# Optimization experiments

Hardware: AMD Instinct MI355X
Metric: run time of the kernel (lower is better)

Reference implementation:

```python
import jax, jax.numpy as jnp
import numpy as np

N_HEAD = 16

def setup_inputs() -> dict:
    key = jax.random.key(0)
    ks = jax.random.split(key, 5)
    B, S, C = 4, 2048, 1024
    x = jax.random.normal(ks[0], (B, S, C), dtype=jnp.float32)
    w_qkv = jax.random.normal(ks[1], (C, 3 * C), dtype=jnp.float32) * (1.0 / np.sqrt(C))
    b_qkv = jnp.zeros((3 * C,), dtype=jnp.float32)
    w_proj = jax.random.normal(ks[2], (C, C), dtype=jnp.float32) * (1.0 / np.sqrt(C))
    b_proj = jnp.zeros((C,), dtype=jnp.float32)
    return {"x": x, "w_qkv": w_qkv, "b_qkv": b_qkv, "w_proj": w_proj, "b_proj": b_proj}

def reference(x, w_qkv, b_qkv, w_proj, b_proj):
    B, S, C = x.shape
    H = N_HEAD
    D = C // H
    qkv = x @ w_qkv + b_qkv                       # [B,S,3C]
    q, k, v = jnp.split(qkv, 3, axis=-1)
    # [B,S,C] -> [B,H,S,D]
    q = q.reshape(B, S, H, D).transpose(0, 2, 1, 3)
    k = k.reshape(B, S, H, D).transpose(0, 2, 1, 3)
    v = v.reshape(B, S, H, D).transpose(0, 2, 1, 3)
    scores = jnp.einsum('bhqd,bhkd->bhqk', q, k) / jnp.sqrt(jnp.float32(D))
    causal = jnp.tril(jnp.ones((S, S), dtype=bool))
    scores = jnp.where(causal[None, None], scores, -jnp.inf)
    weights = jax.nn.softmax(scores, axis=-1)     # dropout p=0 -> identity
    out = jnp.einsum('bhqk,bhkd->bhqd', weights, v)
    out = out.transpose(0, 2, 1, 3).reshape(B, S, C)
    return out @ w_proj + b_proj
```

## Files before the change

kernel.cpp:

```cpp
#include <hip/hip_runtime.h>

#define SDIM 2048
#define CDIM 1024
#define BDIM 4
#define HDIM 16
#define DDIM 64

#define ATT_SCALE 0.18033688011112042f

typedef __attribute__((ext_vector_type(8))) short bf16x8;
typedef __attribute__((ext_vector_type(4))) short bf16x4;
typedef __attribute__((ext_vector_type(4))) float f32x4;
typedef unsigned short u16;

#define MFMA __builtin_amdgcn_mfma_f32_16x16x32_bf16
#define LDS_ORDER_FENCE() __asm__ __volatile__("" ::: "memory")

#define TILE_BAR()                                                            \
    LDS_ORDER_FENCE();                                                        \
    __builtin_amdgcn_s_barrier();                                             \
    LDS_ORDER_FENCE()

__device__ __forceinline__ u16 f2b(float f) {
    union { float f; unsigned u; } v; v.f = f;
    unsigned r = v.u + 0x7FFFu + ((v.u >> 16) & 1u);
    return (u16)(r >> 16);
}
__device__ __forceinline__ u16 f2b_trunc(float f) {
    union { float f; unsigned u; } v; v.f = f;
    return (u16)(v.u >> 16);
}

typedef const __attribute__((address_space(1))) unsigned int* gas_t;
typedef __attribute__((address_space(3))) unsigned int* las_t;
__device__ __forceinline__ void cp16(const void* g, void* l) {
    __builtin_amdgcn_global_load_lds((gas_t)g, (las_t)l, 16, 0, 0);
}

__device__ __forceinline__ float fast_exp2(float x) {
#if __has_builtin(__builtin_amdgcn_exp2f)
    return __builtin_amdgcn_exp2f(x);
#else
    return __exp2f(x);
#endif
}

__global__ __launch_bounds__(256) void prep(
    const float* __restrict__ x, const float* __restrict__ w_qkv,
    const float* __restrict__ w_proj,
    u16* __restrict__ Xb, u16* __restrict__ WqT, u16* __restrict__ WpT)
{
    __shared__ __align__(16) u16 t[64][72];
    const int bx = blockIdx.x;
    const int tid = threadIdx.x;

    if (bx < 4096) {
        int i = (bx * 256 + tid) * 8;
        float4 a = *reinterpret_cast<const float4*>(&x[i]);
        float4 b = *reinterpret_cast<const float4*>(&x[i + 4]);
        u16 u[8];
        u[0]=f2b(a.x); u[1]=f2b(a.y); u[2]=f2b(a.z); u[3]=f2b(a.w);
        u[4]=f2b(b.x); u[5]=f2b(b.y); u[6]=f2b(b.z); u[7]=f2b(b.w);
        *reinterpret_cast<uint4*>(&Xb[i]) = *reinterpret_cast<uint4*>(u);
        return;
    }

    const float* src; u16* dst; int N, n0, k0;
    if (bx < 4096 + 768) {
        int b2 = bx - 4096;
        src = w_qkv; dst = WqT; N = 3 * CDIM;
        n0 = (b2 % 48) * 64; k0 = (b2 / 48) * 64;
    } else {
        int b2 = bx - 4864;
        src = w_proj; dst = WpT; N = CDIM;
        n0 = (b2 % 16) * 64; k0 = (b2 / 16) * 64;
    }
    const int K = CDIM;
#pragma unroll
    for (int it = 0; it < 4; it++) {
        int c = tid + it * 256;
        int r = c >> 4, c4 = (c & 15) * 4;
        float4 f = *reinterpret_cast<const float4*>(&src[(size_t)(k0 + r) * N + n0 + c4]);
        t[c4 + 0][r] = f2b(f.x);
        t[c4 + 1][r] = f2b(f.y);
        t[c4 + 2][r] = f2b(f.z);
        t[c4 + 3][r] = f2b(f.w);
    }
    __syncthreads();
#pragma unroll
    for (int it = 0; it < 2; it++) {
        int c = tid + it * 256;
        int r = c >> 3, c8 = (c & 7) * 8;
        *reinterpret_cast<uint4*>(&dst[(size_t)(n0 + r) * K + k0 + c8]) =
            *reinterpret_cast<const uint4*>(&t[r][c8]);
    }
}

__global__ __launch_bounds__(256, 2) void gemm_qkv(
    const u16* __restrict__ A, const u16* __restrict__ Bt,
    const float* __restrict__ bias,
    u16* __restrict__ Qb, u16* __restrict__ Kb, u16* __restrict__ Vtb)
{
    __shared__ __align__(16) u16 smem[3 * 8192 + 3 * 4096];
    u16* const AsAll = smem;
    u16* const BsAll = smem + 3 * 8192;

    const int tid = threadIdx.x, lane = tid & 63, wave = tid >> 6;
    const int wm = wave >> 1, wn = wave & 1;
    const int l16 = lane & 15, quad = lane >> 4;
    const int bid = blockIdx.x;
    const int w = (bid & 7) * 96 + (bid >> 3);
    const int bx = w % 24, by = w / 24;
    const int m0 = by * 256, n0 = bx * 128;
    const int K = CDIM;

    const int su = (tid & 7) ^ ((tid >> 3) & 7);
    const int sr = ((tid >> 3) << 1) | (su >> 2);
    const int sc = su & 3;

    const int uc8 = ((((l16 & 1) << 2) | quad) ^ (l16 >> 1)) * 8;
    const int faB = (wm * 64 + (l16 >> 1)) * 64 + uc8;
    const int fbB = (wn * 32 + (l16 >> 1)) * 64 + uc8;

#define STG_A(sb, k0, s)  cp16(&A [(size_t)(m0 + (s) * 64 + sr) * K + (k0) + sc * 8], \
                               &AsAll[(sb) * 8192 + ((s) * 256 + wave * 64) * 8])
#define STG_B(sb, k0, s)  cp16(&Bt[(size_t)(n0 + (s) * 64 + sr) * K + (k0) + sc * 8], \
                               &BsAll[(sb) * 4096 + ((s) * 256 + wave * 64) * 8])
#define FRA(i) (*reinterpret_cast<const bf16x8*>(&AsB[faB + (i) * 512]))
#define FRB(j) (*reinterpret_cast<const bf16x8*>(&BsB[fbB + (j) * 512]))

    f32x4 acc[8][4];
#pragma unroll
    for (int i = 0; i < 8; i++)
#pragma unroll
        for (int j = 0; j < 4; j++) acc[i][j] = (f32x4){0.f, 0.f, 0.f, 0.f};

    const int NT = K / 32;
    STG_A(0, 0, 0); STG_A(0, 0, 1); STG_A(0, 0, 2); STG_A(0, 0, 3);
    STG_B(0, 0, 0); STG_B(0, 0, 1);
    STG_A(1, 32, 0); STG_A(1, 32, 1); STG_A(1, 32, 2); STG_A(1, 32, 3);
    STG_B(1, 32, 0); STG_B(1, 32, 1);
    __asm__ __volatile__("s_waitcnt vmcnt(6)" ::: "memory");
    TILE_BAR();

    for (int t = 0; t < NT; t++) {
        const int buf = t % 3, sbuf = (t + 2) % 3;
        const int kst = (t + 2) * 32;
        const bool st = (t + 2) < NT;
        const u16* AsB = &AsAll[buf * 8192];
        const u16* BsB = &BsAll[buf * 4096];

        bf16x8 av[8], bv[4];
#pragma unroll
        for (int j = 0; j < 4; j++) bv[j] = FRB(j);
#pragma unroll
        for (int i = 0; i < 8; i++) av[i] = FRA(i);
        if (st) {
            STG_A(sbuf, kst, 0); STG_A(sbuf, kst, 1);
            STG_A(sbuf, kst, 2); STG_A(sbuf, kst, 3);
            STG_B(sbuf, kst, 0); STG_B(sbuf, kst, 1);
        }
#pragma unroll
        for (int i = 0; i < 8; i++)
#pragma unroll
            for (int j = 0; j < 4; j++)
                acc[i][j] = MFMA(av[i], bv[j], acc[i][j], 0, 0, 0);

        if (t < NT - 2) {
            __asm__ __volatile__("s_waitcnt vmcnt(6)" ::: "memory");
        } else if (t == NT - 2) {
            __asm__ __volatile__("s_waitcnt vmcnt(0)" ::: "memory");
        }
        TILE_BAR();
    }
#undef STG_A
#undef STG_B
#undef FRA
#undef FRB

    const int mm0 = m0 + wm * 128;
    const int bidx = mm0 >> 11, s0 = mm0 & 2047;
    const int n_base = n0 + wn * 64;
    u16* eb = &smem[wave * (16 * 68)];
    const int erow = lane >> 2, ec = (lane & 3) * 16;

    if (n0 >= 2 * CDIM) {
        const int h = (n_base - 2 * CDIM) >> 6;
        const size_t gb = ((size_t)(bidx * HDIM + h)) * DDIM * SDIM;
#pragma unroll
        for (int ih = 0; ih < 2; ih++) {
#pragma unroll
            for (int j = 0; j < 4; j++) {
                float bvj = bias[n_base + j * 16 + l16];
                LDS_ORDER_FENCE();
#pragma unroll
                for (int i = 0; i < 4; i++)
#pragma unroll
                    for (int r = 0; r < 4; r++)
                        eb[l16 * 68 + i * 16 + quad * 4 + r] =
                            f2b(acc[ih * 4 + i][j][r] + bvj);
                LDS_ORDER_FENCE();
                union { bf16x4 hp[4]; uint4 u[2]; } pk;
                pk.hp[0] = *reinterpret_cast<const bf16x4*>(&eb[erow * 68 + ec]);
                pk.hp[1] = *reinterpret_cast<const bf16x4*>(&eb[erow * 68 + ec + 4]);
                pk.hp[2] = *reinterpret_cast<const bf16x4*>(&eb[erow * 68 + ec + 8]);
                pk.hp[3] = *reinterpret_cast<const bf16x4*>(&eb[erow * 68 + ec + 12]);
                u16* gp = &Vtb[gb + (size_t)(j * 16 + erow) * SDIM + s0 + ih * 64 + ec];
                *reinterpret_cast<uint4*>(gp)     = pk.u[0];
                *reinterpret_cast<uint4*>(gp + 8) = pk.u[1];
            }
        }
    } else {
        const bool isK = (n_base >= CDIM);
        u16* dst = isK ? Kb : Qb;
        const float scale = isK ? 1.0f : ATT_SCALE;
        const int hh = (n_base & 1023) >> 6;
        const size_t hb = ((size_t)(bidx * HDIM + hh)) * SDIM;
        float bvj[4];
#pragma unroll
        for (int j = 0; j < 4; j++) bvj[j] = bias[n_base + j * 16 + l16];
#pragma unroll
        for (int i = 0; i < 8; i++) {
            LDS_ORDER_FENCE();
#pragma unroll
            for (int j = 0; j < 4; j++)
#pragma unroll
                for (int r = 0; r < 4; r++)
                    eb[(quad * 4 + r) * 68 + j * 16 + l16] =
                        f2b((acc[i][j][r] + bvj[j]) * scale);
            LDS_ORDER_FENCE();
            union { bf16x4 hp[4]; uint4 u[2]; } pk;
            pk.hp[0] = *reinterpret_cast<const bf16x4*>(&eb[erow * 68 + ec]);
            pk.hp[1] = *reinterpret_cast<const bf16x4*>(&eb[erow * 68 + ec + 4]);
            pk.hp[2] = *reinterpret_cast<const bf16x4*>(&eb[erow * 68 + ec + 8]);
            pk.hp[3] = *reinterpret_cast<const bf16x4*>(&eb[erow * 68 + ec + 12]);
            const int s = s0 + i * 16 + erow;
            u16* gp = &dst[(hb + s) * DDIM + ec];
            *reinterpret_cast<uint4*>(gp)     = pk.u[0];
            *reinterpret_cast<uint4*>(gp + 8) = pk.u[1];
        }
    }
}

__global__ __launch_bounds__(512, 4) void attn(
    const u16* __restrict__ Qb, const u16* __restrict__ Kb,
    const u16* __restrict__ Vtb, u16* __restrict__ Ob)
{
    __shared__ __align__(16) u16 Ks[2][64 * 64];
    __shared__ __align__(16) u16 Vts[2][64 * 64];
    __shared__ __align__(16) u16 Ps[8][32 * 68];

    const int tid = threadIdx.x;
    const int lane = tid & 63, wave = tid >> 6;
    const int l16 = lane & 15, quad = lane >> 4;
    const int x = blockIdx.x;
    const int bh = (x & 7) * 8 + ((x >> 3) & 7);
    const int g8 = (x >> 6) & 3;
    const int qt = (x >> 8) ? g8 : (7 - g8);
    const int q0 = qt * 256;
    const int b = bh >> 4, h = bh & 15;
    const size_t base = (size_t)bh * (SDIM * DDIM);

    const int cl0 = wave * 64 + lane;
    const int sr0 = cl0 >> 3, scc = cl0 & 7;
    const int sg0 = scc ^ (sr0 & 7);

    const int qr0 = q0 + wave * 32 + l16;
    bf16x8 aq0 = *reinterpret_cast<const bf16x8*>(&Qb[base + (size_t)qr0 * DDIM + quad * 8]);
    bf16x8 aq1 = *reinterpret_cast<const bf16x8*>(&Qb[base + (size_t)qr0 * DDIM + 32 + quad * 8]);
    const int qr1 = qr0 + 16;
    bf16x8 aq2 = *reinterpret_cast<const bf16x8*>(&Qb[base + (size_t)qr1 * DDIM + quad * 8]);
    bf16x8 aq3 = *reinterpret_cast<const bf16x8*>(&Qb[base + (size_t)qr1 * DDIM + 32 + quad * 8]);

    u16* Pw = &Ps[wave][0];

    f32x4 O[2][4];
    f32x4 Osum[2];
#pragma unroll
    for (int g = 0; g < 2; g++) {
        Osum[g] = (f32x4){0.f, 0.f, 0.f, 0.f};
#pragma unroll
        for (int j = 0; j < 4; j++) O[g][j] = (f32x4){0.f, 0.f, 0.f, 0.f};
    }
    const short onev = (l16 == 0) ? (short)0x3F80 : (short)0;
    const bf16x8 bones = {onev, onev, onev, onev, onev, onev, onev, onev};

    const int nkb = (qt + 1) * 4;
    const int Arow = q0 + wave * 32;

    cp16(&Kb [base + (size_t)sr0 * DDIM + sg0 * 8], &Ks[0][wave * 512]);
    cp16(&Vtb[base + (size_t)sr0 * SDIM + sg0 * 8], &Vts[0][wave * 512]);

    for (int kbi = 0; kbi < nkb; kbi++) {
        const int cur = kbi & 1;
        const int kb = kbi * 64;
        __syncthreads();
        if (kbi + 1 < nkb) {
            const int kb2 = kb + 64;
            cp16(&Kb [base + (size_t)(kb2 + sr0) * DDIM + sg0 * 8], &Ks[1 - cur][wave * 512]);
            cp16(&Vtb[base + (size_t)sr0 * SDIM + kb2 + sg0 * 8], &Vts[1 - cur][wave * 512]);
        }
        if (kb > Arow + 31) continue;

        const u16* Kc = &Ks[cur][0];
        const u16* Vc = &Vts[cur][0];

        f32x4 sc0[4], sc1[4];
#pragma unroll
        for (int j = 0; j < 4; j++) {
            int kr = j * 16 + l16;
            bf16x8 bk0 = *reinterpret_cast<const bf16x8*>(&Kc[(kr * 8 + ( quad      ^ (kr & 7))) * 8]);
            bf16x8 bk1 = *reinterpret_cast<const bf16x8*>(&Kc[(kr * 8 + ((quad + 4) ^ (kr & 7))) * 8]);
            f32x4 s = (f32x4){0.f, 0.f, 0.f, 0.f};
            s = MFMA(aq0, bk0, s, 0, 0, 0);
            s = MFMA(aq1, bk1, s, 0, 0, 0);
            sc0[j] = s;
            s = (f32x4){0.f, 0.f, 0.f, 0.f};
            s = MFMA(aq2, bk0, s, 0, 0, 0);
            s = MFMA(aq3, bk1, s, 0, 0, 0);
            sc1[j] = s;
        }
        if (kb + 63 > Arow) {
            const int qrel0 = Arow - kb;
#pragma unroll
            for (int j = 0; j < 4; j++) {
                int kk = j * 16 + l16;
#pragma unroll
                for (int r = 0; r < 4; r++) {
                    sc0[j][r] = (kk <= qrel0 + quad * 4 + r)      ? sc0[j][r] : -1e30f;
                    sc1[j][r] = (kk <= qrel0 + 16 + quad * 4 + r) ? sc1[j][r] : -1e30f;
                }
            }
        }
#pragma unroll
        for (int j = 0; j < 4; j++)
#pragma unroll
            for (int r = 0; r < 4; r++) {
                Pw[(quad * 4 + r) * 68 + j * 16 + l16]        = f2b_trunc(fast_exp2(sc0[j][r]));
                Pw[(16 + quad * 4 + r) * 68 + j * 16 + l16]   = f2b_trunc(fast_exp2(sc1[j][r]));
            }
        LDS_ORDER_FENCE();
        union { bf16x4 hp[2]; bf16x8 f; } a0u, a1u, a2u, a3u;
        a0u.hp[0] = *reinterpret_cast<const bf16x4*>(&Pw[l16 * 68 + quad * 8]);
        a0u.hp[1] = *reinterpret_cast<const bf16x4*>(&Pw[l16 * 68 + quad * 8 + 4]);
        a1u.hp[0] = *reinterpret_cast<const bf16x4*>(&Pw[l16 * 68 + 32 + quad * 8]);
        a1u.hp[1] = *reinterpret_cast<const bf16x4*>(&Pw[l16 * 68 + 32 + quad * 8 + 4]);
        a2u.hp[0] = *reinterpret_cast<const bf16x4*>(&Pw[(16 + l16) * 68 + quad * 8]);
        a2u.hp[1] = *reinterpret_cast<const bf16x4*>(&Pw[(16 + l16) * 68 + quad * 8 + 4]);
        a3u.hp[0] = *reinterpret_cast<const bf16x4*>(&Pw[(16 + l16) * 68 + 32 + quad * 8]);
        a3u.hp[1] = *reinterpret_cast<const bf16x4*>(&Pw[(16 + l16) * 68 + 32 + quad * 8 + 4]);

#pragma unroll
        for (int j = 0; j < 4; j++) {
            int vr = j * 16 + l16;
            bf16x8 bv0 = *reinterpret_cast<const bf16x8*>(&Vc[(vr * 8 + ( quad      ^ (vr & 7))) * 8]);
            bf16x8 bv1 = *reinterpret_cast<const bf16x8*>(&Vc[(vr * 8 + ((quad + 4) ^ (vr & 7))) * 8]);
            O[0][j] = MFMA(a0u.f, bv0, O[0][j], 0, 0, 0);
            O[0][j] = MFMA(a1u.f, bv1, O[0][j], 0, 0, 0);
            O[1][j] = MFMA(a2u.f, bv0, O[1][j], 0, 0, 0);
            O[1][j] = MFMA(a3u.f, bv1, O[1][j], 0, 0, 0);
        }
        Osum[0] = MFMA(a0u.f, bones, Osum[0], 0, 0, 0);
        Osum[0] = MFMA(a1u.f, bones, Osum[0], 0, 0, 0);
        Osum[1] = MFMA(a2u.f, bones, Osum[1], 0, 0, 0);
        Osum[1] = MFMA(a3u.f, bones, Osum[1], 0, 0, 0);
    }

#pragma unroll
    for (int g = 0; g < 2; g++) {
#pragma unroll
        for (int r = 0; r < 4; r++) {
            float l = __shfl(Osum[g][r], (lane & 48));
            float inv = 1.0f / l;
            int s = q0 + wave * 32 + g * 16 + quad * 4 + r;
#pragma unroll
            for (int j = 0; j < 4; j++)
                Ob[((size_t)(b * SDIM + s)) * CDIM + h * 64 + j * 16 + l16] =
                    f2b(O[g][j][r] * inv);
        }
    }
}

__global__ __launch_bounds__(256, 2) void gemm_proj(
    const u16* __restrict__ A, const u16* __restrict__ Bt,
    const float* __restrict__ bias, float* __restrict__ out)
{
    __shared__ __align__(16) u16 smem[3 * 8192 + 3 * 4096];
    u16* const AsAll = smem;
    u16* const BsAll = smem + 3 * 8192;

    const int tid = threadIdx.x, lane = tid & 63, wave = tid >> 6;
    const int wm = wave >> 1, wn = wave & 1;
    const int l16 = lane & 15, quad = lane >> 4;
    const int bid = blockIdx.x;
    const int w = (bid & 7) * 32 + (bid >> 3);
    const int bx = w & 7, by = w >> 3;
    const int m0 = by * 256, n0 = bx * 128;
    const int K = CDIM, N = CDIM;

    const int su = (tid & 7) ^ ((tid >> 3) & 7);
    const int sr = ((tid >> 3) << 1) | (su >> 2);
    const int sc = su & 3;

    const int uc8 = ((((l16 & 1) << 2) | quad) ^ (l16 >> 1)) * 8;
    const int faB = (wm * 64 + (l16 >> 1)) * 64 + uc8;
    const int fbB = (wn * 32 + (l16 >> 1)) * 64 + uc8;

#define STG_A(sb, k0, s)  cp16(&A [(size_t)(m0 + (s) * 64 + sr) * K + (k0) + sc * 8], \
                               &AsAll[(sb) * 8192 + ((s) * 256 + wave * 64) * 8])
#define STG_B(sb, k0, s)  cp16(&Bt[(size_t)(n0 + (s) * 64 + sr) * K + (k0) + sc * 8], \
                               &BsAll[(sb) * 4096 + ((s) * 256 + wave * 64) * 8])
#define FRA(i) (*reinterpret_cast<const bf16x8*>(&AsB[faB + (i) * 512]))
#define FRB(j) (*reinterpret_cast<const bf16x8*>(&BsB[fbB + (j) * 512]))

    f32x4 acc[8][4];
#pragma unroll
    for (int i = 0; i < 8; i++)
#pragma unroll
        for (int j = 0; j < 4; j++) acc[i][j] = (f32x4){0.f, 0.f, 0.f, 0.f};

    const int NT = K / 32;
    STG_A(0, 0, 0); STG_A(0, 0, 1); STG_A(0, 0, 2); STG_A(0, 0, 3);
    STG_B(0, 0, 0); STG_B(0, 0, 1);
    STG_A(1, 32, 0); STG_A(1, 32, 1); STG_A(1, 32, 2); STG_A(1, 32, 3);
    STG_B(1, 32, 0); STG_B(1, 32, 1);
    __asm__ __volatile__("s_waitcnt vmcnt(6)" ::: "memory");
    TILE_BAR();

    for (int t = 0; t < NT; t++) {
        const int buf = t % 3, sbuf = (t + 2) % 3;
        const int kst = (t + 2) * 32;
        const bool st = (t + 2) < NT;
        const u16* AsB = &AsAll[buf * 8192];
        const u16* BsB = &BsAll[buf * 4096];

        bf16x8 av[8], bv[4];
#pragma unroll
        for (int j = 0; j < 4; j++) bv[j] = FRB(j);
#pragma unroll
        for (int i = 0; i < 8; i++) av[i] = FRA(i);
        if (st) {
            STG_A(sbuf, kst, 0); STG_A(sbuf, kst, 1);
            STG_A(sbuf, kst, 2); STG_A(sbuf, kst, 3);
            STG_B(sbuf, kst, 0); STG_B(sbuf, kst, 1);
        }
#pragma unroll
        for (int i = 0; i < 8; i++)
#pragma unroll
            for (int j = 0; j < 4; j++)
                acc[i][j] = MFMA(av[i], bv[j], acc[i][j], 0, 0, 0);

        if (t < NT - 2) {
            __asm__ __volatile__("s_waitcnt vmcnt(6)" ::: "memory");
        } else if (t == NT - 2) {
            __asm__ __volatile__("s_waitcnt vmcnt(0)" ::: "memory");
        }
        TILE_BAR();
    }
#undef STG_A
#undef STG_B
#undef FRA
#undef FRB

#pragma unroll
    for (int i = 0; i < 8; i++) {
        int mbase = m0 + wm * 128 + i * 16 + quad * 4;
#pragma unroll
        for (int j = 0; j < 4; j++) {
            int n = n0 + wn * 64 + j * 16 + l16;
            float bv = bias[n];
#pragma unroll
            for (int r = 0; r < 4; r++)
                out[(size_t)(mbase + r) * N + n] = acc[i][j][r] + bv;
        }
    }
}

extern "C" void kernel_launch(void* const* d_in, const int* in_sizes, int n_in,
                              void* d_out, int out_size, void* d_ws, size_t ws_size,
                              hipStream_t stream) {
    const float* x      = (const float*)d_in[0];
    const float* w_qkv  = (const float*)d_in[1];
    const float* b_qkv  = (const float*)d_in[2];
    const float* w_proj = (const float*)d_in[3];
    const float* b_proj = (const float*)d_in[4];
    float* out = (float*)d_out;

    const size_t per = (size_t)BDIM * HDIM * SDIM * DDIM;
    u16* Qb  = (u16*)d_ws;
    u16* Kb  = Qb + per;
    u16* Vtb = Kb + per;
    u16* Ob  = Vtb + per;
    u16* Xb  = Ob;
    u16* WqT = Ob + per;
    u16* WpT = WqT + (size_t)3 * CDIM * CDIM;

    prep<<<dim3(4096 + 768 + 256), dim3(256), 0, stream>>>(x, w_qkv, w_proj, Xb, WqT, WpT);

    gemm_qkv<<<dim3(768), dim3(256), 0, stream>>>(Xb, WqT, b_qkv, Qb, Kb, Vtb);
    attn<<<dim3(512), dim3(512), 0, stream>>>(Qb, Kb, Vtb, Ob);
    gemm_proj<<<dim3(256), dim3(256), 0, stream>>>(Ob, WpT, b_proj, out);
}
```

Measured before the change: 231.0 us.

## Deepen GEMM pipeline to four LDS stages with register double-buffered fragments

Both the QKV and output-projection GEMMs go from a 3-stage to a 4-stage LDS ring, prefetching three K-tiles ahead. They also load the next tile's A/B fragments into a second register set while the MFMAs run on the current set. The loop is unrolled by two so the register buffers alternate. The aim is to hide LDS read latency and global load latency behind matrix math. The cost is about 96 KB of shared memory per block, which likely stops two blocks fitting per CU under the stated launch bounds, plus higher VGPR use.

```diff
diff --git a/kernel.cpp b/kernel.cpp
--- a/kernel.cpp
+++ b/kernel.cpp
@@ -101,9 +101,9 @@
     const float* __restrict__ bias,
     u16* __restrict__ Qb, u16* __restrict__ Kb, u16* __restrict__ Vtb)
 {
-    __shared__ __align__(16) u16 smem[3 * 8192 + 3 * 4096];
+    __shared__ __align__(16) u16 smem[4 * 8192 + 4 * 4096];
     u16* const AsAll = smem;
-    u16* const BsAll = smem + 3 * 8192;
+    u16* const BsAll = smem + 4 * 8192;
 
     const int tid = threadIdx.x, lane = tid & 63, wave = tid >> 6;
     const int wm = wave >> 1, wn = wave & 1;
@@ -126,53 +126,65 @@
                                &AsAll[(sb) * 8192 + ((s) * 256 + wave * 64) * 8])
 #define STG_B(sb, k0, s)  cp16(&Bt[(size_t)(n0 + (s) * 64 + sr) * K + (k0) + sc * 8], \
                                &BsAll[(sb) * 4096 + ((s) * 256 + wave * 64) * 8])
-#define FRA(i) (*reinterpret_cast<const bf16x8*>(&AsB[faB + (i) * 512]))
-#define FRB(j) (*reinterpret_cast<const bf16x8*>(&BsB[fbB + (j) * 512]))
+#define FRA(P, i) (*reinterpret_cast<const bf16x8*>(&(P)[faB + (i) * 512]))
+#define FRB(P, j) (*reinterpret_cast<const bf16x8*>(&(P)[fbB + (j) * 512]))
 
     f32x4 acc[8][4];
 #pragma unroll
     for (int i = 0; i < 8; i++)
 #pragma unroll
         for (int j = 0; j < 4; j++) acc[i][j] = (f32x4){0.f, 0.f, 0.f, 0.f};
+
+    bf16x8 fa[2][8], fb[2][4];
 
     const int NT = K / 32;
     STG_A(0, 0, 0); STG_A(0, 0, 1); STG_A(0, 0, 2); STG_A(0, 0, 3);
     STG_B(0, 0, 0); STG_B(0, 0, 1);
     STG_A(1, 32, 0); STG_A(1, 32, 1); STG_A(1, 32, 2); STG_A(1, 32, 3);
     STG_B(1, 32, 0); STG_B(1, 32, 1);
+    STG_A(2, 64, 0); STG_A(2, 64, 1); STG_A(2, 64, 2); STG_A(2, 64, 3);
+    STG_B(2, 64, 0); STG_B(2, 64, 1);
     __asm__ __volatile__("s_waitcnt vmcnt(6)" ::: "memory");
     TILE_BAR();
-
-    for (int t = 0; t < NT; t++) {
-        const int buf = t % 3, sbuf = (t + 2) % 3;
-        const int kst = (t + 2) * 32;
-        const bool st = (t + 2) < NT;
-        const u16* AsB = &AsAll[buf * 8192];
-        const u16* BsB = &BsAll[buf * 4096];
-
-        bf16x8 av[8], bv[4];
-#pragma unroll
-        for (int j = 0; j < 4; j++) bv[j] = FRB(j);
-#pragma unroll
-        for (int i = 0; i < 8; i++) av[i] = FRA(i);
-        if (st) {
-            STG_A(sbuf, kst, 0); STG_A(sbuf, kst, 1);
-            STG_A(sbuf, kst, 2); STG_A(sbuf, kst, 3);
-            STG_B(sbuf, kst, 0); STG_B(sbuf, kst, 1);
-        }
-#pragma unroll
-        for (int i = 0; i < 8; i++)
-#pragma unroll
-            for (int j = 0; j < 4; j++)
-                acc[i][j] = MFMA(av[i], bv[j], acc[i][j], 0, 0, 0);
-
-        if (t < NT - 2) {
-            __asm__ __volatile__("s_waitcnt vmcnt(6)" ::: "memory");
-        } else if (t == NT - 2) {
-            __asm__ __volatile__("s_waitcnt vmcnt(0)" ::: "memory");
-        }
-        TILE_BAR();
-    }
+#pragma unroll
+    for (int j = 0; j < 4; j++) fb[0][j] = FRB(BsAll, j);
+#pragma unroll
+    for (int i = 0; i < 8; i++) fa[0][i] = FRA(AsAll, i);
+
+#define GBODY(b, CUR, NXT)                                                    \
+    {                                                                         \
+        if ((b) + 1 < NT) {                                                   \
+            const u16* AsN = &AsAll[(((b) + 1) & 3) * 8192];                  \
+            const u16* BsN = &BsAll[(((b) + 1) & 3) * 4096];                  \
+            _Pragma("unroll")                                                 \
+            for (int j = 0; j < 4; j++) fb[NXT][j] = FRB(BsN, j);             \
+            _Pragma("unroll")                                                 \
+            for (int i = 0; i < 8; i++) fa[NXT][i] = FRA(AsN, i);             \
+        }                                                                     \
+        if ((b) + 3 < NT) {                                                   \
+            const int sb3 = ((b) + 3) & 3, k3 = ((b) + 3) * 32;               \
+            STG_A(sb3, k3, 0); STG_A(sb3, k3, 1);                             \
+            STG_A(sb3, k3, 2); STG_A(sb3, k3, 3);                             \
+            STG_B(sb3, k3, 0); STG_B(sb3, k3, 1);                             \
+        }                                                                     \
+        _Pragma("unroll")                                                     \
+        for (int i = 0; i < 8; i++)                                           \
+            _Pragma("unroll")                                                 \
+            for (int j = 0; j < 4; j++)                                       \
+                acc[i][j] = MFMA(fa[CUR][i], fb[CUR][j], acc[i][j], 0, 0, 0); \
+        if ((b) <= NT - 4) {                                                  \
+            __asm__ __volatile__("s_waitcnt vmcnt(6)" ::: "memory");          \
+        } else if ((b) == NT - 3) {                                           \
+            __asm__ __volatile__("s_waitcnt vmcnt(0)" ::: "memory");          \
+        }                                                                     \
+        TILE_BAR();                                                           \
+    }
+
+    for (int t = 0; t < NT; t += 2) {
+        GBODY(t, 0, 1);
+        GBODY(t + 1, 1, 0);
+    }
+#undef GBODY
 #undef STG_A
 #undef STG_B
 #undef FRA
@@ -385,9 +397,9 @@
     const u16* __restrict__ A, const u16* __restrict__ Bt,
     const float* __restrict__ bias, float* __restrict__ out)
 {
-    __shared__ __align__(16) u16 smem[3 * 8192 + 3 * 4096];
+    __shared__ __align__(16) u16 smem[4 * 8192 + 4 * 4096];
     u16* const AsAll = smem;
-    u16* const BsAll = smem + 3 * 8192;
+    u16* const BsAll = smem + 4 * 8192;
 
     const int tid = threadIdx.x, lane = tid & 63, wave = tid >> 6;
     const int wm = wave >> 1, wn = wave & 1;
@@ -410,53 +422,65 @@
                                &AsAll[(sb) * 8192 + ((s) * 256 + wave * 64) * 8])
 #define STG_B(sb, k0, s)  cp16(&Bt[(size_t)(n0 + (s) * 64 + sr) * K + (k0) + sc * 8], \
                                &BsAll[(sb) * 4096 + ((s) * 256 + wave * 64) * 8])
-#define FRA(i) (*reinterpret_cast<const bf16x8*>(&AsB[faB + (i) * 512]))
-#define FRB(j) (*reinterpret_cast<const bf16x8*>(&BsB[fbB + (j) * 512]))
+#define FRA(P, i) (*reinterpret_cast<const bf16x8*>(&(P)[faB + (i) * 512]))
+#define FRB(P, j) (*reinterpret_cast<const bf16x8*>(&(P)[fbB + (j) * 512]))
 
     f32x4 acc[8][4];
 #pragma unroll
     for (int i = 0; i < 8; i++)
 #pragma unroll
         for (int j = 0; j < 4; j++) acc[i][j] = (f32x4){0.f, 0.f, 0.f, 0.f};
+
+    bf16x8 fa[2][8], fb[2][4];
 
     const int NT = K / 32;
     STG_A(0, 0, 0); STG_A(0, 0, 1); STG_A(0, 0, 2); STG_A(0, 0, 3);
     STG_B(0, 0, 0); STG_B(0, 0, 1);
     STG_A(1, 32, 0); STG_A(1, 32, 1); STG_A(1, 32, 2); STG_A(1, 32, 3);
     STG_B(1, 32, 0); STG_B(1, 32, 1);
+    STG_A(2, 64, 0); STG_A(2, 64, 1); STG_A(2, 64, 2); STG_A(2, 64, 3);
+    STG_B(2, 64, 0); STG_B(2, 64, 1);
     __asm__ __volatile__("s_waitcnt vmcnt(6)" ::: "memory");
     TILE_BAR();
-
-    for (int t = 0; t < NT; t++) {
-        const int buf = t % 3, sbuf = (t + 2) % 3;
-        const int kst = (t + 2) * 32;
-        const bool st = (t + 2) < NT;
-        const u16* AsB = &AsAll[buf * 8192];
-        const u16* BsB = &BsAll[buf * 4096];
-
-        bf16x8 av[8], bv[4];
-#pragma unroll
-        for (int j = 0; j < 4; j++) bv[j] = FRB(j);
-#pragma unroll
-        for (int i = 0; i < 8; i++) av[i] = FRA(i);
-        if (st) {
-            STG_A(sbuf, kst, 0); STG_A(sbuf, kst, 1);
-            STG_A(sbuf, kst, 2); STG_A(sbuf, kst, 3);
-            STG_B(sbuf, kst, 0); STG_B(sbuf, kst, 1);
-        }
-#pragma unroll
-        for (int i = 0; i < 8; i++)
-#pragma unroll
-            for (int j = 0; j < 4; j++)
-                acc[i][j] = MFMA(av[i], bv[j], acc[i][j], 0, 0, 0);
-
-        if (t < NT - 2) {
-            __asm__ __volatile__("s_waitcnt vmcnt(6)" ::: "memory");
-        } else if (t == NT - 2) {
-            __asm__ __volatile__("s_waitcnt vmcnt(0)" ::: "memory");
-        }
-        TILE_BAR();
-    }
+#pragma unroll
+    for (int j = 0; j < 4; j++) fb[0][j] = FRB(BsAll, j);
+#pragma unroll
+    for (int i = 0; i < 8; i++) fa[0][i] = FRA(AsAll, i);
+
+#define GBODY(b, CUR, NXT)                                                    \
+    {                                                                         \
+        if ((b) + 1 < NT) {                                                   \
+            const u16* AsN = &AsAll[(((b) + 1) & 3) * 8192];                  \
+            const u16* BsN = &BsAll[(((b) + 1) & 3) * 4096];                  \
+            _Pragma("unroll")                                                 \
+            for (int j = 0; j < 4; j++) fb[NXT][j] = FRB(BsN, j);             \
+            _Pragma("unroll")                                                 \
+            for (int i = 0; i < 8; i++) fa[NXT][i] = FRA(AsN, i);             \
+        }                                                                     \
+        if ((b) + 3 < NT) {                                                   \
+            const int sb3 = ((b) + 3) & 3, k3 = ((b) + 3) * 32;               \
+            STG_A(sb3, k3, 0); STG_A(sb3, k3, 1);                             \
+            STG_A(sb3, k3, 2); STG_A(sb3, k3, 3);                             \
+            STG_B(sb3, k3, 0); STG_B(sb3, k3, 1);                             \
+        }                                                                     \
+        _Pragma("unroll")                                                     \
+        for (int i = 0; i < 8; i++)                                           \
+            _Pragma("unroll")                                                 \
+            for (int j = 0; j < 4; j++)                                       \
+                acc[i][j] = MFMA(fa[CUR][i], fb[CUR][j], acc[i][j], 0, 0, 0); \
+        if ((b) <= NT - 4) {                                                  \
+            __asm__ __volatile__("s_waitcnt vmcnt(6)" ::: "memory");          \
+        } else if ((b) == NT - 3) {                                           \
+            __asm__ __volatile__("s_waitcnt vmcnt(0)" ::: "memory");          \
+        }                                                                     \
+        TILE_BAR();                                                           \
+    }
+
+    for (int t = 0; t < NT; t += 2) {
+        GBODY(t, 0, 1);
+        GBODY(t + 1, 1, 0);
+    }
+#undef GBODY
 #undef STG_A
 #undef STG_B
 #undef FRA
```

After: 262.9 us. 13.8% more time.

## Give each attention wave 64 query rows with 4 waves per block

Applied to the files above, without the earlier changes.

The attention kernel moves from 8 waves of 32 query rows each to 4 waves of 64 query rows each, keeping the same 256-row block tile. Each K/V fragment read from LDS now feeds four MFMA row groups instead of two, which cuts LDS traffic per FLOP, and the causal mask plus exp2 is folded into the QK loop per group. The cost is higher register use (more O accumulators and Q fragments), fewer waves per block to hide latency, and a lower occupancy target in the launch bounds.

```diff
diff --git a/kernel.cpp b/kernel.cpp
--- a/kernel.cpp
+++ b/kernel.cpp
@@ -242,13 +242,13 @@
     }
 }
 
-__global__ __launch_bounds__(512, 4) void attn(
+__global__ __launch_bounds__(256, 2) void attn(
     const u16* __restrict__ Qb, const u16* __restrict__ Kb,
     const u16* __restrict__ Vtb, u16* __restrict__ Ob)
 {
     __shared__ __align__(16) u16 Ks[2][64 * 64];
     __shared__ __align__(16) u16 Vts[2][64 * 64];
-    __shared__ __align__(16) u16 Ps[8][32 * 68];
+    __shared__ __align__(16) u16 Ps[4][64 * 68];
 
     const int tid = threadIdx.x;
     const int lane = tid & 63, wave = tid >> 6;
@@ -261,23 +261,23 @@
     const int b = bh >> 4, h = bh & 15;
     const size_t base = (size_t)bh * (SDIM * DDIM);
 
-    const int cl0 = wave * 64 + lane;
-    const int sr0 = cl0 >> 3, scc = cl0 & 7;
+    const int sr0 = tid >> 3, scc = tid & 7;
     const int sg0 = scc ^ (sr0 & 7);
 
-    const int qr0 = q0 + wave * 32 + l16;
-    bf16x8 aq0 = *reinterpret_cast<const bf16x8*>(&Qb[base + (size_t)qr0 * DDIM + quad * 8]);
-    bf16x8 aq1 = *reinterpret_cast<const bf16x8*>(&Qb[base + (size_t)qr0 * DDIM + 32 + quad * 8]);
-    const int qr1 = qr0 + 16;
-    bf16x8 aq2 = *reinterpret_cast<const bf16x8*>(&Qb[base + (size_t)qr1 * DDIM + quad * 8]);
-    bf16x8 aq3 = *reinterpret_cast<const bf16x8*>(&Qb[base + (size_t)qr1 * DDIM + 32 + quad * 8]);
+    bf16x8 aq[4][2];
+#pragma unroll
+    for (int g = 0; g < 4; g++) {
+        const int qr = q0 + wave * 64 + g * 16 + l16;
+        aq[g][0] = *reinterpret_cast<const bf16x8*>(&Qb[base + (size_t)qr * DDIM + quad * 8]);
+        aq[g][1] = *reinterpret_cast<const bf16x8*>(&Qb[base + (size_t)qr * DDIM + 32 + quad * 8]);
+    }
 
     u16* Pw = &Ps[wave][0];
 
-    f32x4 O[2][4];
-    f32x4 Osum[2];
-#pragma unroll
-    for (int g = 0; g < 2; g++) {
+    f32x4 O[4][4];
+    f32x4 Osum[4];
+#pragma unroll
+    for (int g = 0; g < 4; g++) {
         Osum[g] = (f32x4){0.f, 0.f, 0.f, 0.f};
 #pragma unroll
         for (int j = 0; j < 4; j++) O[g][j] = (f32x4){0.f, 0.f, 0.f, 0.f};
@@ -286,10 +286,12 @@
     const bf16x8 bones = {onev, onev, onev, onev, onev, onev, onev, onev};
 
     const int nkb = (qt + 1) * 4;
-    const int Arow = q0 + wave * 32;
-
-    cp16(&Kb [base + (size_t)sr0 * DDIM + sg0 * 8], &Ks[0][wave * 512]);
-    cp16(&Vtb[base + (size_t)sr0 * SDIM + sg0 * 8], &Vts[0][wave * 512]);
+    const int Arow = q0 + wave * 64;
+
+    cp16(&Kb [base + (size_t)sr0 * DDIM + sg0 * 8],        &Ks[0][wave * 512]);
+    cp16(&Kb [base + (size_t)(sr0 + 32) * DDIM + sg0 * 8], &Ks[0][2048 + wave * 512]);
+    cp16(&Vtb[base + (size_t)sr0 * SDIM + sg0 * 8],        &Vts[0][wave * 512]);
+    cp16(&Vtb[base + (size_t)(sr0 + 32) * SDIM + sg0 * 8], &Vts[0][2048 + wave * 512]);
 
     for (int kbi = 0; kbi < nkb; kbi++) {
         const int cur = kbi & 1;
@@ -297,82 +299,76 @@
         __syncthreads();
         if (kbi + 1 < nkb) {
             const int kb2 = kb + 64;
-            cp16(&Kb [base + (size_t)(kb2 + sr0) * DDIM + sg0 * 8], &Ks[1 - cur][wave * 512]);
-            cp16(&Vtb[base + (size_t)sr0 * SDIM + kb2 + sg0 * 8], &Vts[1 - cur][wave * 512]);
-        }
-        if (kb > Arow + 31) continue;
+            cp16(&Kb [base + (size_t)(kb2 + sr0) * DDIM + sg0 * 8],        &Ks[1 - cur][wave * 512]);
+            cp16(&Kb [base + (size_t)(kb2 + sr0 + 32) * DDIM + sg0 * 8],   &Ks[1 - cur][2048 + wave * 512]);
+            cp16(&Vtb[base + (size_t)sr0 * SDIM + kb2 + sg0 * 8],          &Vts[1 - cur][wave * 512]);
+            cp16(&Vtb[base + (size_t)(sr0 + 32) * SDIM + kb2 + sg0 * 8],   &Vts[1 - cur][2048 + wave * 512]);
+        }
+        if (kb > Arow + 63) continue;
 
         const u16* Kc = &Ks[cur][0];
         const u16* Vc = &Vts[cur][0];
-
-        f32x4 sc0[4], sc1[4];
+        const bool diag = (kb + 63 > Arow);
+        const int qrel0 = Arow - kb;
+
 #pragma unroll
         for (int j = 0; j < 4; j++) {
             int kr = j * 16 + l16;
             bf16x8 bk0 = *reinterpret_cast<const bf16x8*>(&Kc[(kr * 8 + ( quad      ^ (kr & 7))) * 8]);
             bf16x8 bk1 = *reinterpret_cast<const bf16x8*>(&Kc[(kr * 8 + ((quad + 4) ^ (kr & 7))) * 8]);
-            f32x4 s = (f32x4){0.f, 0.f, 0.f, 0.f};
-            s = MFMA(aq0, bk0, s, 0, 0, 0);
-            s = MFMA(aq1, bk1, s, 0, 0, 0);
-            sc0[j] = s;
-            s = (f32x4){0.f, 0.f, 0.f, 0.f};
-            s = MFMA(aq2, bk0, s, 0, 0, 0);
-            s = MFMA(aq3, bk1, s, 0, 0, 0);
-            sc1[j] = s;
-        }
-        if (kb + 63 > Arow) {
-            const int qrel0 = Arow - kb;
-#pragma unroll
-            for (int j = 0; j < 4; j++) {
-                int kk = j * 16 + l16;
-#pragma unroll
-                for (int r = 0; r < 4; r++) {
-                    sc0[j][r] = (kk <= qrel0 + quad * 4 + r)      ? sc0[j][r] : -1e30f;
-                    sc1[j][r] = (kk <= qrel0 + 16 + quad * 4 + r) ? sc1[j][r] : -1e30f;
+#pragma unroll
+            for (int g = 0; g < 4; g++) {
+                f32x4 s = (f32x4){0.f, 0.f, 0.f, 0.f};
+                s = MFMA(aq[g][0], bk0, s, 0, 0, 0);
+                s = MFMA(aq[g][1], bk1, s, 0, 0, 0);
+                if (diag) {
+                    int kk = j * 16 + l16;
+#pragma unroll
+                    for (int r = 0; r < 4; r++)
+                        s[r] = (kk <= qrel0 + g * 16 + quad * 4 + r) ? s[r] : -1e30f;
                 }
+#pragma unroll
+                for (int r = 0; r < 4; r++)
+                    Pw[(g * 16 + quad * 4 + r) * 68 + j * 16 + l16] =
+                        f2b_trunc(fast_exp2(s[r]));
             }
         }
-#pragma unroll
-        for (int j = 0; j < 4; j++)
-#pragma unroll
-            for (int r = 0; r < 4; r++) {
-                Pw[(quad * 4 + r) * 68 + j * 16 + l16]        = f2b_trunc(fast_exp2(sc0[j][r]));
-                Pw[(16 + quad * 4 + r) * 68 + j * 16 + l16]   = f2b_trunc(fast_exp2(sc1[j][r]));
-            }
         LDS_ORDER_FENCE();
-        union { bf16x4 hp[2]; bf16x8 f; } a0u, a1u, a2u, a3u;
-        a0u.hp[0] = *reinterpret_cast<const bf16x4*>(&Pw[l16 * 68 + quad * 8]);
-        a0u.hp[1] = *reinterpret_cast<const bf16x4*>(&Pw[l16 * 68 + quad * 8 + 4]);
-        a1u.hp[0] = *reinterpret_cast<const bf16x4*>(&Pw[l16 * 68 + 32 + quad * 8]);
-        a1u.hp[1] = *reinterpret_cast<const bf16x4*>(&Pw[l16 * 68 + 32 + quad * 8 + 4]);
-        a2u.hp[0] = *reinterpret_cast<const bf16x4*>(&Pw[(16 + l16) * 68 + quad * 8]);
-        a2u.hp[1] = *reinterpret_cast<const bf16x4*>(&Pw[(16 + l16) * 68 + quad * 8 + 4]);
-        a3u.hp[0] = *reinterpret_cast<const bf16x4*>(&Pw[(16 + l16) * 68 + 32 + quad * 8]);
-        a3u.hp[1] = *reinterpret_cast<const bf16x4*>(&Pw[(16 + l16) * 68 + 32 + quad * 8 + 4]);
+        union { bf16x4 hp[2]; bf16x8 f; } pa0[4], pa1[4];
+#pragma unroll
+        for (int g = 0; g < 4; g++) {
+            const int prow = (g * 16 + l16) * 68;
+            pa0[g].hp[0] = *reinterpret_cast<const bf16x4*>(&Pw[prow + quad * 8]);
+            pa0[g].hp[1] = *reinterpret_cast<const bf16x4*>(&Pw[prow + quad * 8 + 4]);
+            pa1[g].hp[0] = *reinterpret_cast<const bf16x4*>(&Pw[prow + 32 + quad * 8]);
+            pa1[g].hp[1] = *reinterpret_cast<const bf16x4*>(&Pw[prow + 32 + quad * 8 + 4]);
+        }
 
 #pragma unroll
         for (int j = 0; j < 4; j++) {
             int vr = j * 16 + l16;
             bf16x8 bv0 = *reinterpret_cast<const bf16x8*>(&Vc[(vr * 8 + ( quad      ^ (vr & 7))) * 8]);
             bf16x8 bv1 = *reinterpret_cast<const bf16x8*>(&Vc[(vr * 8 + ((quad + 4) ^ (vr & 7))) * 8]);
-            O[0][j] = MFMA(a0u.f, bv0, O[0][j], 0, 0, 0);
-            O[0][j] = MFMA(a1u.f, bv1, O[0][j], 0, 0, 0);
-            O[1][j] = MFMA(a2u.f, bv0, O[1][j], 0, 0, 0);
-            O[1][j] = MFMA(a3u.f, bv1, O[1][j], 0, 0, 0);
-        }
-        Osum[0] = MFMA(a0u.f, bones, Osum[0], 0, 0, 0);
-        Osum[0] = MFMA(a1u.f, bones, Osum[0], 0, 0, 0);
-        Osum[1] = MFMA(a2u.f, bones, Osum[1], 0, 0, 0);
-        Osum[1] = MFMA(a3u.f, bones, Osum[1], 0, 0, 0);
-    }
-
-#pragma unroll
-    for (int g = 0; g < 2; g++) {
+#pragma unroll
+            for (int g = 0; g < 4; g++) {
+                O[g][j] = MFMA(pa0[g].f, bv0, O[g][j], 0, 0, 0);
+                O[g][j] = MFMA(pa1[g].f, bv1, O[g][j], 0, 0, 0);
+            }
+        }
+#pragma unroll
+        for (int g = 0; g < 4; g++) {
+            Osum[g] = MFMA(pa0[g].f, bones, Osum[g], 0, 0, 0);
+            Osum[g] = MFMA(pa1[g].f, bones, Osum[g], 0, 0, 0);
+        }
+    }
+
+#pragma unroll
+    for (int g = 0; g < 4; g++) {
 #pragma unroll
         for (int r = 0; r < 4; r++) {
             float l = __shfl(Osum[g][r], (lane & 48));
             float inv = 1.0f / l;
-            int s = q0 + wave * 32 + g * 16 + quad * 4 + r;
+            int s = q0 + wave * 64 + g * 16 + quad * 4 + r;
 #pragma unroll
             for (int j = 0; j < 4; j++)
                 Ob[((size_t)(b * SDIM + s)) * CDIM + h * 64 + j * 16 + l16] =
@@ -498,6 +494,6 @@
     prep<<<dim3(4096 + 768 + 256), dim3(256), 0, stream>>>(x, w_qkv, w_proj, Xb, WqT, WpT);
 
     gemm_qkv<<<dim3(768), dim3(256), 0, stream>>>(Xb, WqT, b_qkv, Qb, Kb, Vtb);
-    attn<<<dim3(512), dim3(512), 0, stream>>>(Qb, Kb, Vtb, Ob);
+    attn<<<dim3(512), dim3(256), 0, stream>>>(Qb, Kb, Vtb, Ob);
     gemm_proj<<<dim3(256), dim3(256), 0, stream>>>(Ob, WpT, b_proj, out);
 }
```

Result: slower. 252.4 us (+9.3%).

## Shrink LDS footprint: double-buffer QKV GEMM and halve attention P scratch

Applied to the files above, without the earlier changes.

The QKV GEMM moves from a three-stage to a two-stage LDS pipeline, prefetching one tile ahead and waiting for all loads before each barrier. The attention kernel halves its per-wave P scratch by writing and reading the two 16-row P halves one after the other through the same buffer. Both changes cut shared memory per block, which may allow more resident blocks. The cost is less prefetch depth in the GEMM, so load latency is more exposed, and extra serialization in attention.

```diff
diff --git a/kernel.cpp b/kernel.cpp
--- a/kernel.cpp
+++ b/kernel.cpp
@@ -101,9 +101,9 @@
     const float* __restrict__ bias,
     u16* __restrict__ Qb, u16* __restrict__ Kb, u16* __restrict__ Vtb)
 {
-    __shared__ __align__(16) u16 smem[3 * 8192 + 3 * 4096];
+    __shared__ __align__(16) u16 smem[2 * 8192 + 2 * 4096];
     u16* const AsAll = smem;
-    u16* const BsAll = smem + 3 * 8192;
+    u16* const BsAll = smem + 2 * 8192;
 
     const int tid = threadIdx.x, lane = tid & 63, wave = tid >> 6;
     const int wm = wave >> 1, wn = wave & 1;
@@ -138,15 +138,11 @@
     const int NT = K / 32;
     STG_A(0, 0, 0); STG_A(0, 0, 1); STG_A(0, 0, 2); STG_A(0, 0, 3);
     STG_B(0, 0, 0); STG_B(0, 0, 1);
-    STG_A(1, 32, 0); STG_A(1, 32, 1); STG_A(1, 32, 2); STG_A(1, 32, 3);
-    STG_B(1, 32, 0); STG_B(1, 32, 1);
-    __asm__ __volatile__("s_waitcnt vmcnt(6)" ::: "memory");
+    __asm__ __volatile__("s_waitcnt vmcnt(0)" ::: "memory");
     TILE_BAR();
 
     for (int t = 0; t < NT; t++) {
-        const int buf = t % 3, sbuf = (t + 2) % 3;
-        const int kst = (t + 2) * 32;
-        const bool st = (t + 2) < NT;
+        const int buf = t & 1;
         const u16* AsB = &AsAll[buf * 8192];
         const u16* BsB = &BsAll[buf * 4096];
 
@@ -155,10 +151,11 @@
         for (int j = 0; j < 4; j++) bv[j] = FRB(j);
 #pragma unroll
         for (int i = 0; i < 8; i++) av[i] = FRA(i);
-        if (st) {
-            STG_A(sbuf, kst, 0); STG_A(sbuf, kst, 1);
-            STG_A(sbuf, kst, 2); STG_A(sbuf, kst, 3);
-            STG_B(sbuf, kst, 0); STG_B(sbuf, kst, 1);
+        if (t + 1 < NT) {
+            const int sb = buf ^ 1, kst = (t + 1) * 32;
+            STG_A(sb, kst, 0); STG_A(sb, kst, 1);
+            STG_A(sb, kst, 2); STG_A(sb, kst, 3);
+            STG_B(sb, kst, 0); STG_B(sb, kst, 1);
         }
 #pragma unroll
         for (int i = 0; i < 8; i++)
@@ -166,9 +163,7 @@
             for (int j = 0; j < 4; j++)
                 acc[i][j] = MFMA(av[i], bv[j], acc[i][j], 0, 0, 0);
 
-        if (t < NT - 2) {
-            __asm__ __volatile__("s_waitcnt vmcnt(6)" ::: "memory");
-        } else if (t == NT - 2) {
+        if (t + 1 < NT) {
             __asm__ __volatile__("s_waitcnt vmcnt(0)" ::: "memory");
         }
         TILE_BAR();
@@ -248,7 +243,7 @@
 {
     __shared__ __align__(16) u16 Ks[2][64 * 64];
     __shared__ __align__(16) u16 Vts[2][64 * 64];
-    __shared__ __align__(16) u16 Ps[8][32 * 68];
+    __shared__ __align__(16) u16 Ps[8][16 * 68];
 
     const int tid = threadIdx.x;
     const int lane = tid & 63, wave = tid >> 6;
@@ -332,23 +327,29 @@
                 }
             }
         }
+        union { bf16x4 hp[2]; bf16x8 f; } a0u, a1u, a2u, a3u;
 #pragma unroll
         for (int j = 0; j < 4; j++)
 #pragma unroll
-            for (int r = 0; r < 4; r++) {
-                Pw[(quad * 4 + r) * 68 + j * 16 + l16]        = f2b_trunc(fast_exp2(sc0[j][r]));
-                Pw[(16 + quad * 4 + r) * 68 + j * 16 + l16]   = f2b_trunc(fast_exp2(sc1[j][r]));
-            }
+            for (int r = 0; r < 4; r++)
+                Pw[(quad * 4 + r) * 68 + j * 16 + l16] = f2b_trunc(fast_exp2(sc0[j][r]));
         LDS_ORDER_FENCE();
-        union { bf16x4 hp[2]; bf16x8 f; } a0u, a1u, a2u, a3u;
         a0u.hp[0] = *reinterpret_cast<const bf16x4*>(&Pw[l16 * 68 + quad * 8]);
         a0u.hp[1] = *reinterpret_cast<const bf16x4*>(&Pw[l16 * 68 + quad * 8 + 4]);
         a1u.hp[0] = *reinterpret_cast<const bf16x4*>(&Pw[l16 * 68 + 32 + quad * 8]);
         a1u.hp[1] = *reinterpret_cast<const bf16x4*>(&Pw[l16 * 68 + 32 + quad * 8 + 4]);
-        a2u.hp[0] = *reinterpret_cast<const bf16x4*>(&Pw[(16 + l16) * 68 + quad * 8]);
-        a2u.hp[1] = *reinterpret_cast<const bf16x4*>(&Pw[(16 + l16) * 68 + quad * 8 + 4]);
-        a3u.hp[0] = *reinterpret_cast<const bf16x4*>(&Pw[(16 + l16) * 68 + 32 + quad * 8]);
-        a3u.hp[1] = *reinterpret_cast<const bf16x4*>(&Pw[(16 + l16) * 68 + 32 + quad * 8 + 4]);
+        LDS_ORDER_FENCE();
+#pragma unroll
+        for (int j = 0; j < 4; j++)
+#pragma unroll
+            for (int r = 0; r < 4; r++)
+                Pw[(quad * 4 + r) * 68 + j * 16 + l16] = f2b_trunc(fast_exp2(sc1[j][r]));
+        LDS_ORDER_FENCE();
+        a2u.hp[0] = *reinterpret_cast<const bf16x4*>(&Pw[l16 * 68 + quad * 8]);
+        a2u.hp[1] = *reinterpret_cast<const bf16x4*>(&Pw[l16 * 68 + quad * 8 + 4]);
+        a3u.hp[0] = *reinterpret_cast<const bf16x4*>(&Pw[l16 * 68 + 32 + quad * 8]);
+        a3u.hp[1] = *reinterpret_cast<const bf16x4*>(&Pw[l16 * 68 + 32 + quad * 8 + 4]);
+        LDS_ORDER_FENCE();
 
 #pragma unroll
         for (int j = 0; j < 4; j++) {
```

Result: slower. 246.1 us (+6.5%).
